# Performance work log

Measured on AMD Instinct MI355X. Metric: run time of the kernel, lower is better.

Reference implementation:

```python
import jax, jax.numpy as jnp
import numpy as np

B, S, HID = 2, 4096, 2048
H, KV, D = 16, 4, 128
BS_, L, G, STRIDE, WTOK = 64, 4, 4, 4, 2048
SCALE = float(D) ** -0.5
NEG = -1.0e9


def _rope_tables(seq, dim):
    inv = 1.0 / (10000.0 ** (np.arange(0, dim, 2, dtype=np.float64) / dim))
    f = np.arange(seq, dtype=np.float64)[:, None] * inv[None, :]
    emb = np.concatenate([f, f], axis=-1)
    return np.cos(emb).astype(np.float32), np.sin(emb).astype(np.float32)


def _rotate_half(x):
    x1, x2 = x[..., : x.shape[-1] // 2], x[..., x.shape[-1] // 2 :]
    return jnp.concatenate([-x2, x1], axis=-1)


def _global_idx(nb, g, stride, max_away):
    # static (trace-time) computation of strided global block indices per query block
    g_idx = np.zeros((nb, g), dtype=np.int32)
    g_valid = np.zeros((nb, g), dtype=np.float32)
    for i in range(1, nb):
        cand = np.arange(max(0, i - max_away), i)
        if stride > 1:
            cand = cand[::stride]
        if cand.size == 0:
            continue
        if cand.size > g:
            cand = cand[-g:]
        s0 = g - cand.size
        g_idx[i, s0:] = cand
        g_valid[i, s0:] = 1.0
    return jnp.asarray(g_idx), jnp.asarray(g_valid)


def setup_inputs():
    key = jax.random.key(0)
    ks = jax.random.split(key, 5)
    hidden_states = jax.random.normal(ks[0], (B, S, HID), jnp.float32)
    cos_t, sin_t = _rope_tables(S, D)
    cos = jnp.broadcast_to(jnp.asarray(cos_t)[None], (B, S, D))
    sin = jnp.broadcast_to(jnp.asarray(sin_t)[None], (B, S, D))
    attention_mask_2d = jnp.ones((B, S), jnp.float32)
    sd = HID ** -0.5
    Wq = jax.random.normal(ks[1], (HID, H * D), jnp.float32) * sd
    Wk = jax.random.normal(ks[2], (HID, KV * D), jnp.float32) * sd
    Wv = jax.random.normal(ks[3], (HID, KV * D), jnp.float32) * sd
    Wo = jax.random.normal(ks[4], (H * D, HID), jnp.float32) * sd
    return dict(hidden_states=hidden_states, cos=cos, sin=sin,
                attention_mask_2d=attention_mask_2d, Wq=Wq, Wk=Wk, Wv=Wv, Wo=Wo)


def reference(hidden_states, cos, sin, attention_mask_2d, Wq, Wk, Wv, Wo):
    b, s, _ = hidden_states.shape
    q = (hidden_states @ Wq).reshape(b, s, H, D).transpose(0, 2, 1, 3)   # [b,H,s,d]
    k = (hidden_states @ Wk).reshape(b, s, KV, D).transpose(0, 2, 1, 3)  # [b,KV,s,d]
    v = (hidden_states @ Wv).reshape(b, s, KV, D).transpose(0, 2, 1, 3)
    c, sn = cos[:, None], sin[:, None]
    q = q * c + _rotate_half(q) * sn
    k = k * c + _rotate_half(k) * sn
    rep = H // KV
    k = jnp.repeat(k, rep, axis=1)
    v = jnp.repeat(v, rep, axis=1)

    nb = s // BS_
    qb = q.reshape(b, H, nb, BS_, D)
    kb = k.reshape(b, H, nb, BS_, D)
    vb = v.reshape(b, H, nb, BS_, D)
    km = attention_mask_2d.reshape(b, nb, BS_)

    # local window of L previous-or-current blocks (left-padded with zero blocks)
    pad = L - 1
    kp = jnp.pad(kb, ((0, 0), (0, 0), (pad, 0), (0, 0), (0, 0)))
    vp = jnp.pad(vb, ((0, 0), (0, 0), (pad, 0), (0, 0), (0, 0)))
    kmp = jnp.pad(km, ((0, 0), (pad, 0), (0, 0)))
    k_loc = jnp.stack([kp[:, :, w : w + nb] for w in range(L)], axis=3)   # [b,H,nb,L,BS,d]
    v_loc = jnp.stack([vp[:, :, w : w + nb] for w in range(L)], axis=3)
    km_loc = jnp.stack([kmp[:, w : w + nb] for w in range(L)], axis=2)    # [b,nb,L,BS]

    s_loc = jnp.einsum('bhqtd,bhqwsd->bhqtws', qb, k_loc) * SCALE
    s_loc = s_loc + (1.0 - km_loc)[:, None, :, None] * NEG
    ar = jnp.arange(BS_)
    intra = jnp.where(ar[None, :] > ar[:, None], NEG, 0.0)  # causal inside current block
    s_loc = s_loc.at[:, :, :, :, -1, :].add(intra)

    # strided global blocks
    g_idx, g_valid = _global_idx(nb, G, STRIDE, max(1, WTOK // BS_))
    k_g = kb[:, :, g_idx]   # [b,H,nb,G,BS,d]
    v_g = vb[:, :, g_idx]
    km_g = km[:, g_idx] * g_valid[None, :, :, None]  # [b,nb,G,BS]
    s_g = jnp.einsum('bhqtd,bhqwsd->bhqtws', qb, k_g) * SCALE
    s_g = s_g + (1.0 - km_g)[:, None, :, None] * NEG

    scores = jnp.concatenate([s_loc.reshape(b, H, nb, BS_, L * BS_),
                              s_g.reshape(b, H, nb, BS_, G * BS_)], axis=-1)
    v_all = jnp.concatenate([v_loc.reshape(b, H, nb, L * BS_, D),
                             v_g.reshape(b, H, nb, G * BS_, D)], axis=3)
    probs = jax.nn.softmax(scores, axis=-1)
    out = jnp.einsum('bhqtk,bhqkd->bhqtd', probs, v_all)
    out = out.reshape(b, H, s, D).transpose(0, 2, 1, 3).reshape(b, s, H * D)
    return out @ Wo
```

## Files before the change

### kernel.cpp

```cpp
#include <hip/hip_runtime.h>
#include <hip/hip_bf16.h>

typedef __hip_bfloat16 bf16;
typedef __attribute__((ext_vector_type(8))) short v8s;
typedef __attribute__((ext_vector_type(4))) short v4s;
typedef __attribute__((ext_vector_type(4))) float v4f;

#define MFMA(a, b, c) __builtin_amdgcn_mfma_f32_16x16x32_bf16((a), (b), (c), 0, 0, 0)

static constexpr int BB = 2, SEQ = 4096, HIDN = 2048, NH = 16, NKV = 4, HD = 128;
static constexpr float SCALE = 0.08838834764831845f;
static constexpr float NEGV = -1e9f;

__device__ __forceinline__ bf16 f2b(float x) { return __float2bfloat16(x); }

__device__ __forceinline__ unsigned int packbf2(float a, float b) {
  union { bf16 h; unsigned short u; } ua, ub;
  ua.h = f2b(a); ub.h = f2b(b);
  return (unsigned int)ua.u | ((unsigned int)ub.u << 16);
}

__device__ __forceinline__ void glds16(const bf16* g, bf16* l) {
  __builtin_amdgcn_global_load_lds(
      (const __attribute__((address_space(1))) unsigned int*)g,
      (__attribute__((address_space(3))) unsigned int*)l, 16, 0, 0);
}

__global__ void convert_k(const float* __restrict__ X, bf16* __restrict__ Y, long n) {
  long i4 = ((long)blockIdx.x * 256 + threadIdx.x) * 4;
  if (i4 >= n) return;
  v4f x = *(const v4f*)(X + i4);
  bf16 t[4];
#pragma unroll
  for (int j = 0; j < 4; j++) t[j] = f2b(x[j]);
  *(v4s*)(Y + i4) = *(const v4s*)t;
}

__global__ __launch_bounds__(256) void transpose_k(const float* __restrict__ W,
                                                   bf16* __restrict__ Wt,
                                                   int K, int N) {
  __shared__ bf16 tile[64][65];
  const int tx = threadIdx.x & 63, ty = threadIdx.x >> 6;
  const int k0 = blockIdx.y << 6, n0 = blockIdx.x << 6;
#pragma unroll
  for (int rr = 0; rr < 64; rr += 4)
    tile[tx][rr + ty] = f2b(W[(long)(k0 + rr + ty) * N + n0 + tx]);
  __syncthreads();
#pragma unroll
  for (int rr = 0; rr < 64; rr += 4)
    Wt[(long)(n0 + rr + ty) * K + k0 + tx] = tile[rr + ty][tx];
}

template <int MODE, typename OT>
__global__ __launch_bounds__(256) void gemm128(const bf16* __restrict__ A,
                                               const bf16* __restrict__ Bt,
                                               OT* __restrict__ C,
                                               int M, int N, int K) {
  __shared__ __align__(16) bf16 As[2][128 * 32];
  __shared__ __align__(16) bf16 Bs[2][128 * 32];

  const int tid = threadIdx.x;
  const int lane = tid & 63, wv = tid >> 6;
  const int wr = wv >> 1, wc = wv & 1;
  const int l15 = lane & 15, quad = lane >> 4;
  const int m0 = blockIdx.y * 128, n0 = blockIdx.x * 128;

  const bf16* aSrc = A + (long)(m0 + (tid >> 2)) * K + (tid & 3) * 8;
  const bf16* bSrc = Bt + (long)(n0 + (tid >> 2)) * K + (tid & 3) * 8;
  const long rowStride = (long)64 * K;

  int aoff[4], boff[4];
#pragma unroll
  for (int t = 0; t < 4; t++) {
    aoff[t] = (wr * 64 + t * 16 + l15) * 32 + quad * 8;
    boff[t] = (wc * 64 + t * 16 + l15) * 32 + quad * 8;
  }

  v4f acc[4][4];
#pragma unroll
  for (int i = 0; i < 4; i++)
#pragma unroll
    for (int j = 0; j < 4; j++) acc[i][j] = {0.f, 0.f, 0.f, 0.f};

  const int nIter = K >> 5;
  for (int it = 0; it < nIter; ++it) {
    const int kc = it << 5;
    const int bsel = it & 1;
    bf16* aD = As[bsel] + wv * 512;
    bf16* bD = Bs[bsel] + wv * 512;
    glds16(aSrc + kc, aD);
    glds16(aSrc + rowStride + kc, aD + 2048);
    glds16(bSrc + kc, bD);
    glds16(bSrc + rowStride + kc, bD + 2048);
    asm volatile("s_waitcnt vmcnt(0)" ::: "memory");
    __syncthreads();

    const bf16* Ab = As[bsel];
    const bf16* Bb = Bs[bsel];
    v8s af[4], bfv[4];
#pragma unroll
    for (int t = 0; t < 4; t++) {
      af[t] = *(const v8s*)(Ab + aoff[t]);
      bfv[t] = *(const v8s*)(Bb + boff[t]);
    }
#pragma unroll
    for (int i = 0; i < 4; i++)
#pragma unroll
      for (int j = 0; j < 4; j++) acc[i][j] = MFMA(af[i], bfv[j], acc[i][j]);
  }

#pragma unroll
  for (int i = 0; i < 4; i++)
#pragma unroll
    for (int j = 0; j < 4; j++)
#pragma unroll
      for (int r = 0; r < 4; r++) {
        int m = m0 + wr * 64 + i * 16 + quad * 4 + r;
        int n = n0 + wc * 64 + j * 16 + l15;
        long addr;
        if (MODE == 0) {
          addr = (long)m * N + n;
        } else {
          int bb = m >> 12, s = m & (SEQ - 1);
          int hh = n >> 7, d = n & (HD - 1);
          if (MODE == 1)      addr = ((long)(bb * NH + hh) * SEQ + s) * HD + d;
          else if (MODE == 2) addr = ((long)(bb * NKV + hh) * SEQ + s) * HD + d;
          else                addr = ((long)(bb * NKV + hh) * HD + d) * SEQ + s;
        }
        float v = acc[i][j][r];
        if constexpr (sizeof(OT) == 2) C[addr] = f2b(v);
        else                           C[addr] = v;
      }
}

__global__ void rope_k(bf16* __restrict__ X, const float* __restrict__ cs,
                       const float* __restrict__ sn, int nheads) {
  int idx = blockIdx.x * 256 + threadIdx.x;
  int d = idx & 63;
  int row = idx >> 6;
  int s = row & (SEQ - 1);
  int bh = row >> 12;
  int b = bh / nheads;
  long xo = (long)row * HD;
  long co = ((long)b * SEQ + s) * HD;
  float x1 = __bfloat162float(X[xo + d]), x2 = __bfloat162float(X[xo + d + 64]);
  float c1 = cs[co + d], c2 = cs[co + d + 64];
  float s1 = sn[co + d], s2 = sn[co + d + 64];
  X[xo + d] = f2b(x1 * c1 - x2 * s1);
  X[xo + d + 64] = f2b(x2 * c2 + x1 * s2);
}

__global__ __launch_bounds__(256, 3) void attn_k(const bf16* __restrict__ Q,
                                                 const bf16* __restrict__ K,
                                                 const bf16* __restrict__ V,
                                                 const float* __restrict__ msk,
                                                 bf16* __restrict__ ctx) {
  const int i = blockIdx.x >> 2, j = blockIdx.x & 3;
  const int kv = blockIdx.y, b = blockIdx.z;
  const int lane = threadIdx.x & 63, wv = threadIdx.x >> 6;
  const int h = kv * 4 + wv;
  const int l15 = lane & 15, quad = lane >> 4;

  __shared__ __align__(16) bf16 kvs[2][8192];
  __shared__ __align__(16) unsigned short pb[4][16][72];

  int kb[8];
  bool kval[8];
#pragma unroll
  for (int w = 0; w < 4; w++) { kb[w] = i - 3 + w; kval[w] = (kb[w] >= 0); }
  {
    int st = i - 32; if (st < 0) st = 0;
    int n = i - st;
    int cnt = (n + 3) >> 2;
#pragma unroll
    for (int t = 0; t < 4; t++) {
      int jj = cnt + t - 4;
      kval[4 + t] = (jj >= 0);
      kb[4 + t] = (jj >= 0) ? (st + 4 * jj) : 0;
    }
  }
  int kbc[8];
#pragma unroll
  for (int t = 0; t < 8; t++) kbc[t] = kb[t] < 0 ? 0 : kb[t];

  const bf16* qp = Q + ((long)(b * NH + h) * SEQ + i * 64 + j * 16 + l15) * HD + quad * 8;
  v8s qf[4];
#pragma unroll
  for (int kk = 0; kk < 4; kk++) qf[kk] = *(const v8s*)(qp + kk * 32);

  const int klr = lane >> 4, kgp = lane & 15;
  const int vlr = lane >> 3, vgp = lane & 7;

  const bf16* gk = K + (long)(b * NKV + kv) * SEQ * HD;
  const bf16* gv = V + (long)(b * NKV + kv) * HD * SEQ;

  auto stageK = [&](int blk, bf16* dst) {
    const bf16* kbase = gk + (long)blk * 64 * HD;
#pragma unroll
    for (int c = 0; c < 4; c++) {
      int tl = wv * 16 + c * 4 + klr;
      int g = kgp ^ (tl & 15);
      glds16(kbase + (long)tl * HD + g * 8, dst + (wv * 16 + c * 4) * 128);
    }
  };
  auto stageV = [&](int blk, bf16* dst) {
    const bf16* vbase = gv + (long)blk * 64;
#pragma unroll
    for (int c = 0; c < 4; c++) {
      int row = wv * 32 + c * 8 + vlr;
      int g = vgp ^ (row & 7);
      glds16(vbase + (long)row * SEQ + g * 8, dst + (wv * 32 + c * 8) * 64);
    }
  };

  float rmax[4] = {-3.4e38f, -3.4e38f, -3.4e38f, -3.4e38f};

  stageK(kbc[0], kvs[0]);
  asm volatile("s_waitcnt vmcnt(0)" ::: "memory");
  __syncthreads();

  for (int it = 0; it < 8; ++it) {
    const int bsel = it & 1;
    if (it < 7) stageK(kbc[it + 1], kvs[bsel ^ 1]);
    const bf16* Kb = kvs[bsel];
    __builtin_amdgcn_s_setprio(1);
#pragma unroll
    for (int t = 0; t < 4; t++) {
      v4f a = {0.f, 0.f, 0.f, 0.f};
#pragma unroll
      for (int kk = 0; kk < 4; kk++) {
        int off = (t * 16 + l15) * 128 + (((kk * 4 + quad) ^ l15) * 8);
        a = MFMA(qf[kk], *(const v8s*)(Kb + off), a);
      }
#pragma unroll
      for (int r = 0; r < 4; r++) rmax[r] = fmaxf(rmax[r], a[r]);
    }
    __builtin_amdgcn_s_setprio(0);
    __syncthreads();
  }

#pragma unroll
  for (int m = 1; m <= 8; m <<= 1)
#pragma unroll
    for (int r = 0; r < 4; r++) rmax[r] = fmaxf(rmax[r], __shfl_xor(rmax[r], m, 64));
  float mrow[4];
#pragma unroll
  for (int r = 0; r < 4; r++) mrow[r] = rmax[r] * SCALE;

  unsigned int p16[8][8];
  float rsum[4] = {0.f, 0.f, 0.f, 0.f};

  stageK(kbc[0], kvs[0]);
  asm volatile("s_waitcnt vmcnt(0)" ::: "memory");
  __syncthreads();

#pragma unroll
  for (int it = 0; it < 8; ++it) {
    const int bsel = it & 1;
    if (it < 7) stageK(kbc[it + 1], kvs[bsel ^ 1]);
    const bf16* Kb = kvs[bsel];
    __builtin_amdgcn_s_setprio(1);
#pragma unroll
    for (int t = 0; t < 4; t++) {
      v4f a = {0.f, 0.f, 0.f, 0.f};
#pragma unroll
      for (int kk = 0; kk < 4; kk++) {
        int off = (t * 16 + l15) * 128 + (((kk * 4 + quad) ^ l15) * 8);
        a = MFMA(qf[kk], *(const v8s*)(Kb + off), a);
      }
      int tokc = kbc[it] * 64 + t * 16 + l15;
      float madd = kval[it] ? (1.0f - msk[b * SEQ + tokc]) * NEGV : NEGV;
#pragma unroll
      for (int r = 0; r < 4; r++) {
        float x = a[r] * SCALE + madd;
        if (it == 3) {
          int kpp = t * 16 + l15;
          int qpp = j * 16 + quad * 4 + r;
          if (kpp > qpp) x += NEGV;
        }
        float e = __expf(x - mrow[r]);
        rsum[r] += e;
        a[r] = e;
      }
      p16[it][t * 2 + 0] = packbf2(a[0], a[1]);
      p16[it][t * 2 + 1] = packbf2(a[2], a[3]);
    }
    __builtin_amdgcn_s_setprio(0);
    __syncthreads();
  }

#pragma unroll
  for (int m = 1; m <= 8; m <<= 1)
#pragma unroll
    for (int r = 0; r < 4; r++) rsum[r] += __shfl_xor(rsum[r], m, 64);

  v4f oacc[8] = {{0.f, 0.f, 0.f, 0.f}, {0.f, 0.f, 0.f, 0.f}, {0.f, 0.f, 0.f, 0.f},
                 {0.f, 0.f, 0.f, 0.f}, {0.f, 0.f, 0.f, 0.f}, {0.f, 0.f, 0.f, 0.f},
                 {0.f, 0.f, 0.f, 0.f}, {0.f, 0.f, 0.f, 0.f}};

  stageV(kbc[0], kvs[0]);
  asm volatile("s_waitcnt vmcnt(0)" ::: "memory");
  __syncthreads();

#pragma unroll
  for (int it = 0; it < 8; ++it) {
    const int bsel = it & 1;
    if (it < 7) stageV(kbc[it + 1], kvs[bsel ^ 1]);

#pragma unroll
    for (int t = 0; t < 4; t++)
#pragma unroll
      for (int r = 0; r < 4; r++) {
        unsigned int pr = p16[it][t * 2 + (r >> 1)];
        unsigned short u = (r & 1) ? (unsigned short)(pr >> 16)
                                   : (unsigned short)(pr & 0xffff);
        pb[wv][quad * 4 + r][t * 16 + l15] = u;
      }

    const bf16* Vb = kvs[bsel];
    __builtin_amdgcn_s_setprio(1);
#pragma unroll
    for (int hf = 0; hf < 2; hf++) {
      v8s af = *(const v8s*)&pb[wv][l15][hf * 32 + quad * 8];
#pragma unroll
      for (int nt = 0; nt < 8; nt++) {
        int off = (nt * 16 + l15) * 64 + (((hf * 4 + quad) ^ (l15 & 7)) * 8);
        oacc[nt] = MFMA(af, *(const v8s*)(Vb + off), oacc[nt]);
      }
    }
    __builtin_amdgcn_s_setprio(0);
    __syncthreads();
  }

  const int tokw = i * 64 + j * 16 + quad * 4;
#pragma unroll
  for (int nt = 0; nt < 8; nt++)
#pragma unroll
    for (int r = 0; r < 4; r++) {
      float v = oacc[nt][r] / rsum[r];
      long addr = ((long)b * SEQ + tokw + r) * (NH * HD) + h * HD + nt * 16 + l15;
      ctx[addr] = f2b(v);
    }
}

extern "C" void kernel_launch(void* const* d_in, const int* in_sizes, int n_in,
                              void* d_out, int out_size, void* d_ws, size_t ws_size,
                              hipStream_t stream) {
  const float* hs  = (const float*)d_in[0];
  const float* cs  = (const float*)d_in[1];
  const float* sn  = (const float*)d_in[2];
  const float* msk = (const float*)d_in[3];
  const float* Wq  = (const float*)d_in[4];
  const float* Wk  = (const float*)d_in[5];
  const float* Wv  = (const float*)d_in[6];
  const float* Wo  = (const float*)d_in[7];
  float* out = (float*)d_out;

  char* w = (char*)d_ws;
  bf16* hsb = (bf16*)w; w += (size_t)BB * SEQ * HIDN * 2;
  bf16* Wqt = (bf16*)w; w += (size_t)2048 * 2048 * 2;
  bf16* Wkt = (bf16*)w; w += (size_t)512 * 2048 * 2;
  bf16* Wvt = (bf16*)w; w += (size_t)512 * 2048 * 2;
  bf16* Wot = (bf16*)w; w += (size_t)2048 * 2048 * 2;
  bf16* Qr  = (bf16*)w; w += (size_t)BB * NH * SEQ * HD * 2;
  bf16* Kr  = (bf16*)w; w += (size_t)BB * NKV * SEQ * HD * 2;
  bf16* Vt  = (bf16*)w; w += (size_t)BB * NKV * HD * SEQ * 2;
  bf16* ctx = hsb;

  long nhs = (long)BB * SEQ * HIDN;
  convert_k<<<(int)(nhs / 4 / 256), 256, 0, stream>>>(hs, hsb, nhs);

  transpose_k<<<dim3(2048 / 64, 2048 / 64), 256, 0, stream>>>(Wq, Wqt, 2048, 2048);
  transpose_k<<<dim3(512 / 64, 2048 / 64), 256, 0, stream>>>(Wk, Wkt, 2048, 512);
  transpose_k<<<dim3(512 / 64, 2048 / 64), 256, 0, stream>>>(Wv, Wvt, 2048, 512);
  transpose_k<<<dim3(2048 / 64, 2048 / 64), 256, 0, stream>>>(Wo, Wot, 2048, 2048);

  gemm128<1, bf16><<<dim3(2048 / 128, 8192 / 128), 256, 0, stream>>>(hsb, Wqt, Qr, 8192, 2048, 2048);
  gemm128<2, bf16><<<dim3(512 / 128, 8192 / 128), 256, 0, stream>>>(hsb, Wkt, Kr, 8192, 512, 2048);
  gemm128<3, bf16><<<dim3(512 / 128, 8192 / 128), 256, 0, stream>>>(hsb, Wvt, Vt, 8192, 512, 2048);

  rope_k<<<(BB * NH * SEQ * 64) / 256, 256, 0, stream>>>(Qr, cs, sn, NH);
  rope_k<<<(BB * NKV * SEQ * 64) / 256, 256, 0, stream>>>(Kr, cs, sn, NKV);

  attn_k<<<dim3(256, 4, 2), 256, 0, stream>>>(Qr, Kr, Vt, msk, ctx);

  gemm128<0, float><<<dim3(2048 / 128, 8192 / 128), 256, 0, stream>>>(ctx, Wot, out, 8192, 2048, 2048);
}
```

Before: 606.0 us.

## Fuse three-pass block-sparse attention into single online-softmax pass; swizzle GEMM block order

The attention kernel used to make three passes over the selected KV blocks: one QK pass for the row max, a second QK pass for exp and sum, then a PV pass. These are merged into one pass that uses an online softmax with running max and rescaling, and K and V tiles are now staged together into separate double buffers. This removes one full QK recomputation and two extra rounds of K/V staging. In exchange it doubles LDS use, lowers the occupancy hint from 3 to 2 blocks per CU, and adds a per-block rescale of the output accumulators. The GEMM also remaps block IDs with a mod-8 interleave, likely meant to spread neighbouring tiles across XCDs for better cache locality.

```diff
diff --git a/kernel.cpp b/kernel.cpp
--- a/kernel.cpp
+++ b/kernel.cpp
@@ -13,12 +13,6 @@
 static constexpr float NEGV = -1e9f;
 
 __device__ __forceinline__ bf16 f2b(float x) { return __float2bfloat16(x); }
-
-__device__ __forceinline__ unsigned int packbf2(float a, float b) {
-  union { bf16 h; unsigned short u; } ua, ub;
-  ua.h = f2b(a); ub.h = f2b(b);
-  return (unsigned int)ua.u | ((unsigned int)ub.u << 16);
-}
 
 __device__ __forceinline__ void glds16(const bf16* g, bf16* l) {
   __builtin_amdgcn_global_load_lds(
@@ -63,7 +57,11 @@
   const int lane = tid & 63, wv = tid >> 6;
   const int wr = wv >> 1, wc = wv & 1;
   const int l15 = lane & 15, quad = lane >> 4;
-  const int m0 = blockIdx.y * 128, n0 = blockIdx.x * 128;
+
+  const int nwg = gridDim.x * gridDim.y;
+  int bid = blockIdx.y * gridDim.x + blockIdx.x;
+  bid = (bid & 7) * (nwg >> 3) + (bid >> 3);
+  const int m0 = (bid / gridDim.x) * 128, n0 = (bid % gridDim.x) * 128;
 
   const bf16* aSrc = A + (long)(m0 + (tid >> 2)) * K + (tid & 3) * 8;
   const bf16* bSrc = Bt + (long)(n0 + (tid >> 2)) * K + (tid & 3) * 8;
@@ -150,7 +148,7 @@
   X[xo + d + 64] = f2b(x2 * c2 + x1 * s2);
 }
 
-__global__ __launch_bounds__(256, 3) void attn_k(const bf16* __restrict__ Q,
+__global__ __launch_bounds__(256, 2) void attn_k(const bf16* __restrict__ Q,
                                                  const bf16* __restrict__ K,
                                                  const bf16* __restrict__ V,
                                                  const float* __restrict__ msk,
@@ -161,8 +159,9 @@
   const int h = kv * 4 + wv;
   const int l15 = lane & 15, quad = lane >> 4;
 
-  __shared__ __align__(16) bf16 kvs[2][8192];
-  __shared__ __align__(16) unsigned short pb[4][16][72];
+  __shared__ __align__(16) bf16 kbuf[2][8192];
+  __shared__ __align__(16) bf16 vbuf[2][8192];
+  __shared__ __align__(16) bf16 pb[4][16][72];
 
   int kb[8];
   bool kval[8];
@@ -213,77 +212,94 @@
     }
   };
 
-  float rmax[4] = {-3.4e38f, -3.4e38f, -3.4e38f, -3.4e38f};
-
-  stageK(kbc[0], kvs[0]);
+  float m_run[4] = {-3.4e38f, -3.4e38f, -3.4e38f, -3.4e38f};
+  float rsum[4] = {0.f, 0.f, 0.f, 0.f};
+  v4f oacc[8] = {{0.f, 0.f, 0.f, 0.f}, {0.f, 0.f, 0.f, 0.f}, {0.f, 0.f, 0.f, 0.f},
+                 {0.f, 0.f, 0.f, 0.f}, {0.f, 0.f, 0.f, 0.f}, {0.f, 0.f, 0.f, 0.f},
+                 {0.f, 0.f, 0.f, 0.f}, {0.f, 0.f, 0.f, 0.f}};
+
+  stageK(kbc[0], kbuf[0]);
+  stageV(kbc[0], vbuf[0]);
   asm volatile("s_waitcnt vmcnt(0)" ::: "memory");
   __syncthreads();
 
+#pragma unroll
   for (int it = 0; it < 8; ++it) {
     const int bsel = it & 1;
-    if (it < 7) stageK(kbc[it + 1], kvs[bsel ^ 1]);
-    const bf16* Kb = kvs[bsel];
+    if (it < 7) {
+      stageK(kbc[it + 1], kbuf[bsel ^ 1]);
+      stageV(kbc[it + 1], vbuf[bsel ^ 1]);
+    }
+
+    const bf16* Kb = kbuf[bsel];
+    v4f a[4];
     __builtin_amdgcn_s_setprio(1);
 #pragma unroll
     for (int t = 0; t < 4; t++) {
-      v4f a = {0.f, 0.f, 0.f, 0.f};
+      v4f acc = {0.f, 0.f, 0.f, 0.f};
 #pragma unroll
       for (int kk = 0; kk < 4; kk++) {
         int off = (t * 16 + l15) * 128 + (((kk * 4 + quad) ^ l15) * 8);
-        a = MFMA(qf[kk], *(const v8s*)(Kb + off), a);
-      }
-#pragma unroll
-      for (int r = 0; r < 4; r++) rmax[r] = fmaxf(rmax[r], a[r]);
+        acc = MFMA(qf[kk], *(const v8s*)(Kb + off), acc);
+      }
+      a[t] = acc;
     }
     __builtin_amdgcn_s_setprio(0);
-    __syncthreads();
-  }
-
-#pragma unroll
-  for (int m = 1; m <= 8; m <<= 1)
-#pragma unroll
-    for (int r = 0; r < 4; r++) rmax[r] = fmaxf(rmax[r], __shfl_xor(rmax[r], m, 64));
-  float mrow[4];
-#pragma unroll
-  for (int r = 0; r < 4; r++) mrow[r] = rmax[r] * SCALE;
-
-  unsigned int p16[8][8];
-  float rsum[4] = {0.f, 0.f, 0.f, 0.f};
-
-  stageK(kbc[0], kvs[0]);
-  asm volatile("s_waitcnt vmcnt(0)" ::: "memory");
-  __syncthreads();
-
-#pragma unroll
-  for (int it = 0; it < 8; ++it) {
-    const int bsel = it & 1;
-    if (it < 7) stageK(kbc[it + 1], kvs[bsel ^ 1]);
-    const bf16* Kb = kvs[bsel];
-    __builtin_amdgcn_s_setprio(1);
+
+    float bmax[4] = {-3.4e38f, -3.4e38f, -3.4e38f, -3.4e38f};
 #pragma unroll
     for (int t = 0; t < 4; t++) {
-      v4f a = {0.f, 0.f, 0.f, 0.f};
-#pragma unroll
-      for (int kk = 0; kk < 4; kk++) {
-        int off = (t * 16 + l15) * 128 + (((kk * 4 + quad) ^ l15) * 8);
-        a = MFMA(qf[kk], *(const v8s*)(Kb + off), a);
-      }
       int tokc = kbc[it] * 64 + t * 16 + l15;
       float madd = kval[it] ? (1.0f - msk[b * SEQ + tokc]) * NEGV : NEGV;
 #pragma unroll
       for (int r = 0; r < 4; r++) {
-        float x = a[r] * SCALE + madd;
+        float x = a[t][r] * SCALE + madd;
         if (it == 3) {
           int kpp = t * 16 + l15;
           int qpp = j * 16 + quad * 4 + r;
           if (kpp > qpp) x += NEGV;
         }
-        float e = __expf(x - mrow[r]);
+        a[t][r] = x;
+        bmax[r] = fmaxf(bmax[r], x);
+      }
+    }
+#pragma unroll
+    for (int m = 1; m <= 8; m <<= 1)
+#pragma unroll
+      for (int r = 0; r < 4; r++) bmax[r] = fmaxf(bmax[r], __shfl_xor(bmax[r], m, 64));
+
+    float scl[4];
+#pragma unroll
+    for (int r = 0; r < 4; r++) {
+      float nm = fmaxf(m_run[r], bmax[r]);
+      scl[r] = __expf(m_run[r] - nm);
+      m_run[r] = nm;
+      rsum[r] *= scl[r];
+    }
+#pragma unroll
+    for (int nt = 0; nt < 8; nt++)
+#pragma unroll
+      for (int r = 0; r < 4; r++) oacc[nt][r] *= scl[r];
+
+#pragma unroll
+    for (int t = 0; t < 4; t++)
+#pragma unroll
+      for (int r = 0; r < 4; r++) {
+        float e = __expf(a[t][r] - m_run[r]);
         rsum[r] += e;
-        a[r] = e;
-      }
-      p16[it][t * 2 + 0] = packbf2(a[0], a[1]);
-      p16[it][t * 2 + 1] = packbf2(a[2], a[3]);
+        pb[wv][quad * 4 + r][t * 16 + l15] = f2b(e);
+      }
+
+    const bf16* Vb = vbuf[bsel];
+    __builtin_amdgcn_s_setprio(1);
+#pragma unroll
+    for (int hf = 0; hf < 2; hf++) {
+      v8s af = *(const v8s*)&pb[wv][l15][hf * 32 + quad * 8];
+#pragma unroll
+      for (int nt = 0; nt < 8; nt++) {
+        int off = (nt * 16 + l15) * 64 + (((hf * 4 + quad) ^ (l15 & 7)) * 8);
+        oacc[nt] = MFMA(af, *(const v8s*)(Vb + off), oacc[nt]);
+      }
     }
     __builtin_amdgcn_s_setprio(0);
     __syncthreads();
@@ -293,44 +309,6 @@
   for (int m = 1; m <= 8; m <<= 1)
 #pragma unroll
     for (int r = 0; r < 4; r++) rsum[r] += __shfl_xor(rsum[r], m, 64);
-
-  v4f oacc[8] = {{0.f, 0.f, 0.f, 0.f}, {0.f, 0.f, 0.f, 0.f}, {0.f, 0.f, 0.f, 0.f},
-                 {0.f, 0.f, 0.f, 0.f}, {0.f, 0.f, 0.f, 0.f}, {0.f, 0.f, 0.f, 0.f},
-                 {0.f, 0.f, 0.f, 0.f}, {0.f, 0.f, 0.f, 0.f}};
-
-  stageV(kbc[0], kvs[0]);
-  asm volatile("s_waitcnt vmcnt(0)" ::: "memory");
-  __syncthreads();
-
-#pragma unroll
-  for (int it = 0; it < 8; ++it) {
-    const int bsel = it & 1;
-    if (it < 7) stageV(kbc[it + 1], kvs[bsel ^ 1]);
-
-#pragma unroll
-    for (int t = 0; t < 4; t++)
-#pragma unroll
-      for (int r = 0; r < 4; r++) {
-        unsigned int pr = p16[it][t * 2 + (r >> 1)];
-        unsigned short u = (r & 1) ? (unsigned short)(pr >> 16)
-                                   : (unsigned short)(pr & 0xffff);
-        pb[wv][quad * 4 + r][t * 16 + l15] = u;
-      }
-
-    const bf16* Vb = kvs[bsel];
-    __builtin_amdgcn_s_setprio(1);
-#pragma unroll
-    for (int hf = 0; hf < 2; hf++) {
-      v8s af = *(const v8s*)&pb[wv][l15][hf * 32 + quad * 8];
-#pragma unroll
-      for (int nt = 0; nt < 8; nt++) {
-        int off = (nt * 16 + l15) * 64 + (((hf * 4 + quad) ^ (l15 & 7)) * 8);
-        oacc[nt] = MFMA(af, *(const v8s*)(Vb + off), oacc[nt]);
-      }
-    }
-    __builtin_amdgcn_s_setprio(0);
-    __syncthreads();
-  }
 
   const int tokw = i * 64 + j * 16 + quad * 4;
 #pragma unroll
```

Result: faster. 570.7 us (-5.8%).
